# Optimization experiments

Hardware: AMD Instinct MI355X
Metric: run time of the kernel (lower is better)

## Reference

```python
import jax, jax.numpy as jnp
import numpy as np

D_MODEL = 1024
NUM_HEADS = 16
HEAD_DIM = D_MODEL // NUM_HEADS


def setup_inputs() -> dict:
    key = jax.random.key(0)
    kx, kq, kk, kv, ko = jax.random.split(key, 5)
    B, T = 2, 2048
    scale = 1.0 / np.sqrt(D_MODEL)
    return {
        "x": jax.random.normal(kx, (B, T, D_MODEL), dtype=jnp.float32),
        "wq": jax.random.normal(kq, (D_MODEL, D_MODEL), dtype=jnp.float32) * scale,
        "wk": jax.random.normal(kk, (D_MODEL, D_MODEL), dtype=jnp.float32) * scale,
        "wv": jax.random.normal(kv, (D_MODEL, D_MODEL), dtype=jnp.float32) * scale,
        "wo": jax.random.normal(ko, (D_MODEL, D_MODEL), dtype=jnp.float32) * scale,
    }


def _split_heads(x):
    b, t, _ = x.shape
    return x.reshape(b, t, NUM_HEADS, HEAD_DIM).transpose(0, 2, 1, 3)  # [b,h,t,d]


def reference(x, wq, wk, wv, wo):
    q = _split_heads(x @ wq)
    k = _split_heads(x @ wk)
    v = _split_heads(x @ wv)
    inv_sqrt_d = jnp.asarray(1.0 / np.sqrt(HEAD_DIM), x.dtype)
    scores = jnp.einsum("bhqd,bhkd->bhqk", q, k) * inv_sqrt_d
    weights = jax.nn.softmax(scores, axis=-1)  # dropout rate 0.0 -> identity
    out = jnp.einsum("bhqk,bhkd->bhqd", weights, v)
    b, h, t, d = out.shape
    out = out.transpose(0, 2, 1, 3).reshape(b, t, D_MODEL)
    return out @ wo
```

## Files before the change

kernel.cpp:

```cpp
#include <hip/hip_runtime.h>
#include <stdint.h>

using bf16   = __bf16;
using bf16x8 = __bf16 __attribute__((ext_vector_type(8)));
using bf16x4 = __bf16 __attribute__((ext_vector_type(4)));
using f32x4  = float  __attribute__((ext_vector_type(4)));
using f32x16 = float  __attribute__((ext_vector_type(16)));
using u32x4  = uint32_t __attribute__((ext_vector_type(4)));

#define DM 1024
#define T_ 2048
#define NH 16

__device__ __forceinline__ void gl_lds16(const void* g, void* l) {
  __builtin_amdgcn_global_load_lds(
      (__attribute__((address_space(1))) void*)g,
      (__attribute__((address_space(3))) void*)l, 16, 0, 0);
}

__device__ __forceinline__ f32x4 mfma16(bf16x8 a, bf16x8 b, f32x4 c) {
  return __builtin_amdgcn_mfma_f32_16x16x32_bf16(a, b, c, 0, 0, 0);
}
__device__ __forceinline__ f32x16 mfma32(bf16x8 a, bf16x8 b, f32x16 c) {
  return __builtin_amdgcn_mfma_f32_32x32x16_bf16(a, b, c, 0, 0, 0);
}
__device__ __forceinline__ uint32_t cvtpk(float lo, float hi) {
  uint32_t r;
  asm volatile("v_cvt_pk_bf16_f32 %0, %1, %2" : "=v"(r) : "v"(lo), "v"(hi));
  return r;
}

__global__ __launch_bounds__(256)
void k_cast_x(const float* __restrict__ x, bf16* __restrict__ xb) {
  const size_t i = (size_t)blockIdx.x * 256 + threadIdx.x;
  const float4 a = *(const float4*)(x + i * 8);
  const float4 c = *(const float4*)(x + i * 8 + 4);
  bf16x8 v;
  v[0] = (bf16)a.x; v[1] = (bf16)a.y; v[2] = (bf16)a.z; v[3] = (bf16)a.w;
  v[4] = (bf16)c.x; v[5] = (bf16)c.y; v[6] = (bf16)c.z; v[7] = (bf16)c.w;
  *(bf16x8*)(xb + i * 8) = v;
}

__global__ __launch_bounds__(256)
void k_transpose_w4(const float* __restrict__ w0, const float* __restrict__ w1,
                    const float* __restrict__ w2, const float* __restrict__ w3,
                    bf16* __restrict__ wtq, bf16* __restrict__ wto) {
  const int z = blockIdx.z;
  const float* w = (z == 0) ? w0 : (z == 1) ? w1 : (z == 2) ? w2 : w3;
  bf16* wt = (z < 3) ? (wtq + (size_t)z * 1024 * 1024) : wto;
  const float scale = (z == 0) ? 0.125f * 1.44269504f : 1.0f;
  __shared__ float tile[64][68];
  const int tx = threadIdx.x & 15;
  const int ty = threadIdx.x >> 4;
  const int k0 = blockIdx.y * 64, n0 = blockIdx.x * 64;
#pragma unroll
  for (int j = 0; j < 4; ++j) {
    const int r = ty + 16 * j;
    const float4 v = *(const float4*)(w + (size_t)(k0 + r) * DM + n0 + tx * 4);
    tile[r][tx * 4 + 0] = v.x; tile[r][tx * 4 + 1] = v.y;
    tile[r][tx * 4 + 2] = v.z; tile[r][tx * 4 + 3] = v.w;
  }
  __syncthreads();
#pragma unroll
  for (int j = 0; j < 4; ++j) {
    const int r = ty + 16 * j;
    bf16x4 o;
    o[0] = (bf16)(tile[tx * 4 + 0][r] * scale);
    o[1] = (bf16)(tile[tx * 4 + 1][r] * scale);
    o[2] = (bf16)(tile[tx * 4 + 2][r] * scale);
    o[3] = (bf16)(tile[tx * 4 + 3][r] * scale);
    *(bf16x4*)(wt + (size_t)(n0 + r) * DM + k0 + tx * 4) = o;
  }
}

template<int MODE>
__global__ __launch_bounds__(256)
void k_gemm(const bf16* __restrict__ A, const bf16* __restrict__ BT,
            bf16* __restrict__ Qg, bf16* __restrict__ Kg, bf16* __restrict__ Vt,
            float* __restrict__ Cout) {
  constexpr int BN = (MODE == 0) ? 128 : 64;
  constexpr int NTW = BN / 32;
  __shared__ __align__(16) bf16 Ash[128 * 32];
  __shared__ __align__(16) bf16 Bsh[BN * 32];
  const int tn = blockIdx.x, tm = blockIdx.y;
  const int lane = threadIdx.x & 63, w = threadIdx.x >> 6;
  const int wm = w >> 1, wn = w & 1;
  const int r16 = lane & 15, g = lane >> 4;
  f32x4 acc[4][NTW] = {};
  const bf16* Arow = A + (size_t)tm * 128 * DM;
  const bf16* Brow = BT + (size_t)tn * BN * DM;
  for (int k0 = 0; k0 < DM; k0 += 32) {
#pragma unroll
    for (int t = 0; t < 2; ++t) {
      const int q = t * 256 + w * 64 + lane;
      gl_lds16(Arow + (size_t)(q >> 2) * DM + k0 + (q & 3) * 8, Ash + (t * 256 + w * 64) * 8);
    }
#pragma unroll
    for (int t = 0; t < BN / 64; ++t) {
      const int q = t * 256 + w * 64 + lane;
      gl_lds16(Brow + (size_t)(q >> 2) * DM + k0 + (q & 3) * 8, Bsh + (t * 256 + w * 64) * 8);
    }
    __syncthreads();
    bf16x8 af[4], bfr[NTW];
#pragma unroll
    for (int mt = 0; mt < 4; ++mt)
      af[mt] = *(const bf16x8*)(Ash + (wm * 64 + mt * 16 + r16) * 32 + g * 8);
#pragma unroll
    for (int nt = 0; nt < NTW; ++nt)
      bfr[nt] = *(const bf16x8*)(Bsh + (wn * (BN / 2) + nt * 16 + r16) * 32 + g * 8);
#pragma unroll
    for (int mt = 0; mt < 4; ++mt)
#pragma unroll
      for (int nt = 0; nt < NTW; ++nt)
        acc[mt][nt] = mfma16(af[mt], bfr[nt], acc[mt][nt]);
    __syncthreads();
  }
#pragma unroll
  for (int mt = 0; mt < 4; ++mt) {
#pragma unroll
    for (int nt = 0; nt < NTW; ++nt) {
      const int ncol = tn * BN + wn * (BN / 2) + nt * 16 + r16;
      const int m0 = tm * 128 + wm * 64 + mt * 16 + g * 4;
      if (MODE == 0) {
        const int which = ncol >> 10, nl = ncol & 1023;
        const int h = nl >> 6, d = nl & 63;
        const int b = m0 >> 11, t0 = m0 & 2047;
        if (which == 2) {
          bf16x4 pv;
#pragma unroll
          for (int r = 0; r < 4; ++r) pv[r] = (bf16)acc[mt][nt][r];
          *(bf16x4*)(Vt + ((size_t)(b * NH + h) * 64 + d) * T_ + t0) = pv;
        } else {
          bf16* dst = (which == 0) ? Qg : Kg;
#pragma unroll
          for (int r = 0; r < 4; ++r)
            dst[(((size_t)(b * NH + h) * T_ + t0 + r) << 6) + d] = (bf16)acc[mt][nt][r];
        }
      } else {
#pragma unroll
        for (int r = 0; r < 4; ++r)
          Cout[(size_t)(m0 + r) * DM + ncol] = acc[mt][nt][r];
      }
    }
  }
}

__global__ __launch_bounds__(256)
void k_attn(const bf16* __restrict__ Qg, const bf16* __restrict__ Kg,
            const bf16* __restrict__ Vtr, bf16* __restrict__ Ao) {
  __shared__ __align__(16) bf16 Ksh[2][64 * 64];
  __shared__ __align__(16) bf16 Vsh[2][64 * 64];
  const int qt = blockIdx.x, bh = blockIdx.y;
  const int lane = threadIdx.x & 63, w = threadIdx.x >> 6;
  const int l31 = lane & 31, hi = lane >> 5;
  const bf16* Qb = Qg + (size_t)bh * T_ * 64;
  const bf16* Kb = Kg + (size_t)bh * T_ * 64;
  const bf16* Vb = Vtr + (size_t)bh * 64 * T_;
  const int q0 = qt * 128 + w * 32;
  bf16x8 qb[4];
#pragma unroll
  for (int s = 0; s < 4; ++s)
    qb[s] = *(const bf16x8*)(Qb + (size_t)(q0 + l31) * 64 + s * 16 + hi * 8);
  f32x16 o0 = {}, o1 = {};
  float llocal = 0.f;
  const int swz31 = (l31 & 7) << 4;
  const int srow = lane >> 3;
  const int schunk = (lane & 7) ^ srow;

  auto stage = [&](bf16* kbuf, bf16* vbuf, int kt0) {
#pragma unroll
    for (int j = 0; j < 2; ++j) {
      const int idx = w * 2 + j;
      const int row = idx * 8 + srow;
      gl_lds16(Kb + (size_t)(kt0 + row) * 64 + schunk * 8, kbuf + idx * 512);
      gl_lds16(Vb + (size_t)row * T_ + kt0 + schunk * 8, vbuf + idx * 512);
    }
  };

  stage(Ksh[0], Vsh[0], 0);
  __syncthreads();
  constexpr int NT = T_ / 64;
  for (int kt = 0; kt < NT; ++kt) {
    const int cur = kt & 1;
    if (kt + 1 < NT) stage(Ksh[cur ^ 1], Vsh[cur ^ 1], (kt + 1) * 64);
    const char* Kc = (const char*)Ksh[cur];
    const char* Vc = (const char*)Vsh[cur];
    f32x16 st0 = {}, st1 = {};
    __builtin_amdgcn_s_setprio(1);
#pragma unroll
    for (int s = 0; s < 4; ++s) {
      const int cb = (s * 32 + hi * 16) ^ swz31;
      const bf16x8 k0 = *(const bf16x8*)(Kc + l31 * 128 + cb);
      const bf16x8 k1 = *(const bf16x8*)(Kc + (32 + l31) * 128 + cb);
      st0 = mfma32(k0, qb[s], st0);
      st1 = mfma32(k1, qb[s], st1);
    }
    __builtin_amdgcn_s_setprio(0);
#pragma unroll
    for (int r = 0; r < 16; ++r) {
      st0[r] = __builtin_amdgcn_exp2f(st0[r]); llocal += st0[r];
    }
#pragma unroll
    for (int r = 0; r < 16; ++r) {
      st1[r] = __builtin_amdgcn_exp2f(st1[r]); llocal += st1[r];
    }
    __builtin_amdgcn_s_setprio(1);
#pragma unroll
    for (int s = 0; s < 4; ++s) {
      const f32x16& sv = (s < 2) ? st0 : st1;
      const int si = (s & 1) * 8;
      uint32_t a0 = cvtpk(sv[si + 0], sv[si + 1]);
      uint32_t a1 = cvtpk(sv[si + 2], sv[si + 3]);
      uint32_t b0 = cvtpk(sv[si + 4], sv[si + 5]);
      uint32_t b1 = cvtpk(sv[si + 6], sv[si + 7]);
      asm volatile("v_permlane32_swap_b32 %0, %1" : "+v"(a0), "+v"(b0));
      asm volatile("v_permlane32_swap_b32 %0, %1" : "+v"(a1), "+v"(b1));
      u32x4 fr; fr[0] = a0; fr[1] = a1; fr[2] = b0; fr[3] = b1;
      const bf16x8 pas = __builtin_bit_cast(bf16x8, fr);
      const int cb = (s * 32 + hi * 16) ^ swz31;
      const bf16x8 v0 = *(const bf16x8*)(Vc + l31 * 128 + cb);
      const bf16x8 v1 = *(const bf16x8*)(Vc + (32 + l31) * 128 + cb);
      o0 = mfma32(pas, v0, o0);
      o1 = mfma32(pas, v1, o1);
    }
    __builtin_amdgcn_s_setprio(0);
    __syncthreads();
  }
  llocal += __shfl_xor(llocal, 32);
  const int b = bh >> 4, h = bh & 15;
#pragma unroll
  for (int r = 0; r < 16; ++r) {
    const int qoff = (r & 3) + 8 * (r >> 2) + 4 * hi;
    const float linv = 1.f / __shfl(llocal, qoff);
    const size_t base = ((size_t)(b * T_ + q0 + qoff)) * DM + h * 64 + l31;
    Ao[base]      = (bf16)(o0[r] * linv);
    Ao[base + 32] = (bf16)(o1[r] * linv);
  }
}

extern "C" void kernel_launch(void* const* d_in, const int* in_sizes, int n_in,
                              void* d_out, int out_size, void* d_ws, size_t ws_size,
                              hipStream_t stream) {
  const float* x  = (const float*)d_in[0];
  const float* wq = (const float*)d_in[1];
  const float* wk = (const float*)d_in[2];
  const float* wv = (const float*)d_in[3];
  const float* wo = (const float*)d_in[4];
  char* ws = (char*)d_ws;
  const size_t MB = 1024 * 1024;
  bf16* xb   = (bf16*)(ws + 0);
  bf16* wtq  = (bf16*)(ws + 8 * MB);
  bf16* wto  = (bf16*)(ws + 14 * MB);
  bf16* Qg   = (bf16*)(ws + 16 * MB);
  bf16* Kg   = (bf16*)(ws + 24 * MB);
  bf16* Vtr  = (bf16*)(ws + 32 * MB);

  k_cast_x<<<dim3(2048), dim3(256), 0, stream>>>(x, xb);
  k_transpose_w4<<<dim3(16, 16, 4), dim3(256), 0, stream>>>(wq, wk, wv, wo, wtq, wto);
  k_gemm<0><<<dim3(24, 32), dim3(256), 0, stream>>>(xb, wtq, Qg, Kg, Vtr, (float*)nullptr);
  k_attn<<<dim3(16, 32), dim3(256), 0, stream>>>(Qg, Kg, Vtr, xb);
  k_gemm<1><<<dim3(16, 32), dim3(256), 0, stream>>>(xb, wto, (bf16*)nullptr, (bf16*)nullptr,
                                                    (bf16*)nullptr, (float*)d_out);
}
```

Measured before the change: 126.1 us.

## Split attention key range across two wave groups per block and merge via LDS

The attention kernel now runs 512 threads per block. Two groups of four waves each process half of the key sequence for the same 128 queries, each with its own double-buffered K/V tiles. Partial outputs and row sums from the second group are merged into the first group through shared memory before normalization and store. The goal is more in-flight waves per block and a shorter serial key loop per wave, at the cost of double the LDS, an extra reduction step and higher register pressure under the 512 launch bound. The merge just adds the two partials, so it is only correct without a running-max rescale, which matches the existing softmax path.

```diff
diff --git a/kernel.cpp b/kernel.cpp
--- a/kernel.cpp
+++ b/kernel.cpp
@@ -145,18 +145,20 @@
   }
 }
 
-__global__ __launch_bounds__(256)
+__global__ __launch_bounds__(512)
 void k_attn(const bf16* __restrict__ Qg, const bf16* __restrict__ Kg,
             const bf16* __restrict__ Vtr, bf16* __restrict__ Ao) {
-  __shared__ __align__(16) bf16 Ksh[2][64 * 64];
-  __shared__ __align__(16) bf16 Vsh[2][64 * 64];
+  __shared__ __align__(16) bf16 Ksh[2][2][64 * 64];
+  __shared__ __align__(16) bf16 Vsh[2][2][64 * 64];
+  __shared__ float Lsh[4][64];
   const int qt = blockIdx.x, bh = blockIdx.y;
   const int lane = threadIdx.x & 63, w = threadIdx.x >> 6;
+  const int qw = w & 3, kh = w >> 2;
   const int l31 = lane & 31, hi = lane >> 5;
   const bf16* Qb = Qg + (size_t)bh * T_ * 64;
   const bf16* Kb = Kg + (size_t)bh * T_ * 64;
   const bf16* Vb = Vtr + (size_t)bh * 64 * T_;
-  const int q0 = qt * 128 + w * 32;
+  const int q0 = qt * 128 + qw * 32;
   bf16x8 qb[4];
 #pragma unroll
   for (int s = 0; s < 4; ++s)
@@ -167,24 +169,24 @@
   const int srow = lane >> 3;
   const int schunk = (lane & 7) ^ srow;
 
-  auto stage = [&](bf16* kbuf, bf16* vbuf, int kt0) {
+  auto stage = [&](int buf, int ti) {
 #pragma unroll
     for (int j = 0; j < 2; ++j) {
-      const int idx = w * 2 + j;
+      const int idx = qw * 2 + j;
       const int row = idx * 8 + srow;
-      gl_lds16(Kb + (size_t)(kt0 + row) * 64 + schunk * 8, kbuf + idx * 512);
-      gl_lds16(Vb + (size_t)row * T_ + kt0 + schunk * 8, vbuf + idx * 512);
+      gl_lds16(Kb + (size_t)(ti * 64 + row) * 64 + schunk * 8, &Ksh[kh][buf][idx * 512]);
+      gl_lds16(Vb + (size_t)row * T_ + ti * 64 + schunk * 8, &Vsh[kh][buf][idx * 512]);
     }
   };
 
-  stage(Ksh[0], Vsh[0], 0);
+  constexpr int NTH = T_ / 64 / 2;
+  stage(0, kh * NTH);
   __syncthreads();
-  constexpr int NT = T_ / 64;
-  for (int kt = 0; kt < NT; ++kt) {
-    const int cur = kt & 1;
-    if (kt + 1 < NT) stage(Ksh[cur ^ 1], Vsh[cur ^ 1], (kt + 1) * 64);
-    const char* Kc = (const char*)Ksh[cur];
-    const char* Vc = (const char*)Vsh[cur];
+  for (int i = 0; i < NTH; ++i) {
+    const int cur = i & 1;
+    if (i + 1 < NTH) stage(cur ^ 1, kh * NTH + i + 1);
+    const char* Kc = (const char*)Ksh[kh][cur];
+    const char* Vc = (const char*)Vsh[kh][cur];
     f32x16 st0 = {}, st1 = {};
     __builtin_amdgcn_s_setprio(1);
 #pragma unroll
@@ -226,15 +228,33 @@
     __builtin_amdgcn_s_setprio(0);
     __syncthreads();
   }
-  llocal += __shfl_xor(llocal, 32);
-  const int b = bh >> 4, h = bh & 15;
-#pragma unroll
-  for (int r = 0; r < 16; ++r) {
-    const int qoff = (r & 3) + 8 * (r >> 2) + 4 * hi;
-    const float linv = 1.f / __shfl(llocal, qoff);
-    const size_t base = ((size_t)(b * T_ + q0 + qoff)) * DM + h * 64 + l31;
-    Ao[base]      = (bf16)(o0[r] * linv);
-    Ao[base + 32] = (bf16)(o1[r] * linv);
+  float* cb = (float*)&Ksh[0][0][0] + qw * 2048;
+  if (kh == 1) {
+#pragma unroll
+    for (int r = 0; r < 16; ++r) {
+      cb[r * 64 + lane]        = o0[r];
+      cb[(16 + r) * 64 + lane] = o1[r];
+    }
+    Lsh[qw][lane] = llocal;
+  }
+  __syncthreads();
+  if (kh == 0) {
+    llocal += Lsh[qw][lane];
+#pragma unroll
+    for (int r = 0; r < 16; ++r) {
+      o0[r] += cb[r * 64 + lane];
+      o1[r] += cb[(16 + r) * 64 + lane];
+    }
+    llocal += __shfl_xor(llocal, 32);
+    const int b = bh >> 4, h = bh & 15;
+#pragma unroll
+    for (int r = 0; r < 16; ++r) {
+      const int qoff = (r & 3) + 8 * (r >> 2) + 4 * hi;
+      const float linv = 1.f / __shfl(llocal, qoff);
+      const size_t base = ((size_t)(b * T_ + q0 + qoff)) * DM + h * 64 + l31;
+      Ao[base]      = (bf16)(o0[r] * linv);
+      Ao[base + 32] = (bf16)(o1[r] * linv);
+    }
   }
 }
 
@@ -258,7 +278,7 @@
   k_cast_x<<<dim3(2048), dim3(256), 0, stream>>>(x, xb);
   k_transpose_w4<<<dim3(16, 16, 4), dim3(256), 0, stream>>>(wq, wk, wv, wo, wtq, wto);
   k_gemm<0><<<dim3(24, 32), dim3(256), 0, stream>>>(xb, wtq, Qg, Kg, Vtr, (float*)nullptr);
-  k_attn<<<dim3(16, 32), dim3(256), 0, stream>>>(Qg, Kg, Vtr, xb);
+  k_attn<<<dim3(16, 32), dim3(512), 0, stream>>>(Qg, Kg, Vtr, xb);
   k_gemm<1><<<dim3(16, 32), dim3(256), 0, stream>>>(xb, wto, (bf16*)nullptr, (bf16*)nullptr,
                                                     (bf16*)nullptr, (float*)d_out);
 }
```

Result: faster. 122.3 us (-3.0%).
